# Kernel optimization log

Hardware: AMD Instinct MI355X
Metric: run time of the kernel (lower is better)

Reference implementation:

```python
import jax, jax.numpy as jnp
import numpy as np

B, S, HID = 1, 2048, 3072
NH, NKV, HD = 32, 8, 96
N_REP = NH // NKV
ROPE_THETA = 10000.0


def _rotate_half(x):
    half = x.shape[-1] // 2
    return jnp.concatenate([-x[..., half:], x[..., :half]], axis=-1)


def setup_inputs() -> dict:
    key = jax.random.key(0)
    k1, k2, k3 = jax.random.split(key, 3)
    hidden_states = jax.random.normal(k1, (B, S, HID), dtype=jnp.float32)
    qkv_w = jax.random.normal(k2, (NH * HD + 2 * NKV * HD, HID), dtype=jnp.float32) * 0.02
    o_w = jax.random.normal(k3, (HID, NH * HD), dtype=jnp.float32) * 0.02
    position_ids = jnp.broadcast_to(jnp.arange(S, dtype=jnp.int64)[None, :], (B, S))
    causal = jnp.tril(jnp.ones((S, S), dtype=bool))
    attention_mask = jnp.where(causal, 0.0, jnp.finfo(jnp.float32).min)[None, None].astype(jnp.float32)
    attention_mask = jnp.broadcast_to(attention_mask, (B, 1, S, S))
    return {"hidden_states": hidden_states, "position_ids": position_ids,
            "attention_mask": attention_mask, "qkv_w": qkv_w, "o_w": o_w}


def reference(hidden_states, position_ids, attention_mask, qkv_w, o_w):
    b, s, _ = hidden_states.shape
    qkv = jnp.einsum('bsh,oh->bso', hidden_states, qkv_w)
    q_pos = NH * HD
    q = qkv[..., :q_pos]
    k = qkv[..., q_pos:q_pos + NKV * HD]
    v = qkv[..., q_pos + NKV * HD:]
    # [b, heads, s, hd]
    q = q.reshape(b, s, NH, HD).transpose(0, 2, 1, 3)
    k = k.reshape(b, s, NKV, HD).transpose(0, 2, 1, 3)
    v = v.reshape(b, s, NKV, HD).transpose(0, 2, 1, 3)
    # RoPE
    inv_freq = 1.0 / (ROPE_THETA ** (jnp.arange(0, HD, 2, dtype=jnp.float32) / HD))
    freqs = position_ids.astype(jnp.float32)[:, :, None] * inv_freq[None, None, :]  # [b,s,hd/2]
    emb = jnp.concatenate([freqs, freqs], axis=-1)  # [b,s,hd]
    cos = jnp.cos(emb)[:, None, :, :]
    sin = jnp.sin(emb)[:, None, :, :]
    q = q * cos + _rotate_half(q) * sin
    k = k * cos + _rotate_half(k) * sin
    # GQA repeat_kv (repeat_interleave on head dim)
    k = jnp.repeat(k, N_REP, axis=1)
    v = jnp.repeat(v, N_REP, axis=1)
    scores = jnp.einsum('bhqd,bhkd->bhqk', q, k) / jnp.sqrt(jnp.float32(HD))
    scores = scores + attention_mask
    w = jax.nn.softmax(scores.astype(jnp.float32), axis=-1).astype(v.dtype)
    attn = jnp.einsum('bhqk,bhkd->bhqd', w, v)
    attn = attn.transpose(0, 2, 1, 3).reshape(b, s, NH * HD)
    out = jnp.einsum('bsf,of->bso', attn, o_w)
    return out
```

## Files before the change

kernel.cpp:

```cpp
#include <hip/hip_runtime.h>

#define S_LEN 2048
#define HID_DIM 3072
#define NH 32
#define NKV 8
#define HD 96
#define QKV_OUT 4608

typedef __attribute__((ext_vector_type(8))) short short8;
typedef __attribute__((ext_vector_type(4))) float floatx4;

__device__ __forceinline__ unsigned short f2b(float f) {
    unsigned int u = __float_as_uint(f);
    u = (u + 0x7FFFu + ((u >> 16) & 1u)) >> 16;
    return (unsigned short)u;
}
__device__ __forceinline__ float b2f(unsigned short h) {
    return __uint_as_float(((unsigned int)h) << 16);
}
__device__ __forceinline__ void async_ld16(const void* g, void* l) {
    __builtin_amdgcn_global_load_lds((const __attribute__((address_space(1))) void*)g,
                                     (__attribute__((address_space(3))) void*)l, 16, 0, 0);
}
__device__ __forceinline__ float fast_exp2(float x) {
#if __has_builtin(__builtin_amdgcn_exp2f)
    return __builtin_amdgcn_exp2f(x);
#else
    return exp2f(x);
#endif
}
__device__ __forceinline__ void store_out(float* C, size_t i, float v) { C[i] = v; }
__device__ __forceinline__ void store_out(unsigned short* C, size_t i, float v) { C[i] = f2b(v); }


__global__ void cvt3_tiled(const float* __restrict__ a, int nab,
                           const float* __restrict__ b, int nbb,
                           const float* __restrict__ c, int ncb,
                           unsigned short* __restrict__ oa,
                           unsigned short* __restrict__ ob,
                           unsigned short* __restrict__ oc) {
    int wid = blockIdx.x * 4 + (threadIdx.x >> 6);
    const int l = threadIdx.x & 63;
    const float* src;
    unsigned short* dst;
    int j = wid;
    if (j < nab) { src = a; dst = oa; }
    else {
        j -= nab;
        if (j < nbb) { src = b; dst = ob; }
        else {
            j -= nbb;
            if (j >= ncb) return;
            src = c; dst = oc;
        }
    }
    const int KB = HID_DIM >> 5;
    int rt = j / KB, kc = j - rt * KB;
    int i = l & 15, q = l >> 4;
    const float* p = src + ((size_t)rt * 16 + i) * HID_DIM + kc * 32 + q * 8;
    float4 v0 = *(const float4*)p;
    float4 v1 = *(const float4*)(p + 4);
    short8 o;
    o[0] = (short)f2b(v0.x); o[1] = (short)f2b(v0.y);
    o[2] = (short)f2b(v0.z); o[3] = (short)f2b(v0.w);
    o[4] = (short)f2b(v1.x); o[5] = (short)f2b(v1.y);
    o[6] = (short)f2b(v1.z); o[7] = (short)f2b(v1.w);
    *(short8*)(dst + (size_t)j * 512 + l * 8) = o;
}

template <typename OUT>
__global__ void gemm_bt(const unsigned short* __restrict__ A,
                        const unsigned short* __restrict__ B,
                        OUT* __restrict__ C, int M, int N, int K) {
    __shared__ unsigned short As[16 * 512];
    __shared__ unsigned short Bs[16 * 512];
    const int KB = K >> 5;
    const int t = threadIdx.x;
    const int w = t >> 6;
    const int l = t & 63;
    const int lane15 = l & 15;
    const int quad = l >> 4;
    const int rowt = blockIdx.y * 8;
    const int colt = blockIdx.x * 8;
    const int wm = (w >> 1) * 64;
    const int wn = (w & 1) * 64;

    const floatx4 vzero = {0.f, 0.f, 0.f, 0.f};
    floatx4 acc[4][4];
#pragma unroll
    for (int i = 0; i < 4; ++i)
#pragma unroll
        for (int j = 0; j < 4; ++j) acc[i][j] = vzero;

    const int xA = wm >> 4, xB = wn >> 4;
    for (int kc0 = 0; kc0 < KB; kc0 += 2) {
        __syncthreads();
#pragma unroll
        for (int j = 0; j < 4; ++j) {
            int s = w * 4 + j;
            int x = s >> 1, kkb = s & 1;
            size_t ablk = (size_t)(rowt + x) * KB + kc0 + kkb;
            size_t bblk = (size_t)(colt + x) * KB + kc0 + kkb;
            async_ld16(A + ablk * 512 + l * 8, As + s * 512 + l * 8);
            async_ld16(B + bblk * 512 + l * 8, Bs + s * 512 + l * 8);
        }
        __syncthreads();
#pragma unroll
        for (int kkb = 0; kkb < 2; ++kkb) {
            short8 af[4], bfr[4];
#pragma unroll
            for (int mi = 0; mi < 4; ++mi)
                af[mi] = *(const short8*)(As + ((xA + mi) * 2 + kkb) * 512 + l * 8);
#pragma unroll
            for (int ni = 0; ni < 4; ++ni)
                bfr[ni] = *(const short8*)(Bs + ((xB + ni) * 2 + kkb) * 512 + l * 8);
#pragma unroll
            for (int mi = 0; mi < 4; ++mi)
#pragma unroll
                for (int ni = 0; ni < 4; ++ni)
                    acc[mi][ni] = __builtin_amdgcn_mfma_f32_16x16x32_bf16(af[mi], bfr[ni], acc[mi][ni], 0, 0, 0);
        }
    }
#pragma unroll
    for (int mi = 0; mi < 4; ++mi)
#pragma unroll
        for (int ni = 0; ni < 4; ++ni)
#pragma unroll
            for (int r = 0; r < 4; ++r) {
                int m = rowt * 16 + wm + mi * 16 + quad * 4 + r;
                int n = colt * 16 + wn + ni * 16 + lane15;
                store_out(C, (size_t)m * N + n, acc[mi][ni][r]);
            }
}

__global__ void rope_split(const unsigned short* __restrict__ qkv,
                           unsigned short* __restrict__ Qd,
                           unsigned short* __restrict__ Kd,
                           unsigned short* __restrict__ Vd) {
    const int s = blockIdx.x;
    const int t = threadIdx.x;
    const unsigned short* row = qkv + (size_t)s * QKV_OUT;
    const float L2T_48 = 0.2768273412406135f;
    const float SCALE2 = 0.14724444f;

    for (int i = t; i < NH * 48; i += 256) {
        int h = i / 48, d = i - (i / 48) * 48;
        float f = (float)s * exp2f(-(float)d * L2T_48);
        float sn, cs;
        sincosf(f, &sn, &cs);
        float q1 = b2f(row[h * 96 + d]);
        float q2 = b2f(row[h * 96 + d + 48]);
        size_t base = ((size_t)h * S_LEN + s) * HD;
        Qd[base + d] = f2b((q1 * cs - q2 * sn) * SCALE2);
        Qd[base + d + 48] = f2b((q2 * cs + q1 * sn) * SCALE2);
    }
    for (int i = t; i < NKV * 48; i += 256) {
        int h = i / 48, d = i - (i / 48) * 48;
        float f = (float)s * exp2f(-(float)d * L2T_48);
        float sn, cs;
        sincosf(f, &sn, &cs);
        float k1 = b2f(row[3072 + h * 96 + d]);
        float k2 = b2f(row[3072 + h * 96 + d + 48]);
        size_t base = ((size_t)h * S_LEN + s) * HD;
        Kd[base + d] = f2b(k1 * cs - k2 * sn);
        Kd[base + d + 48] = f2b(k2 * cs + k1 * sn);
    }
    for (int i = t; i < NKV * HD; i += 256) {
        int h = i / 96, d = i - (i / 96) * 96;
        Vd[((size_t)h * S_LEN + s) * HD + d] = row[3840 + i];
    }
}

__global__ void transpose_v(const unsigned short* __restrict__ V,
                            unsigned short* __restrict__ Vt) {
    __shared__ unsigned short T[96][72];
    const int kvh = blockIdx.x >> 5;
    const int s0 = (blockIdx.x & 31) * 64;
    const int t = threadIdx.x;
#pragma unroll
    for (int it = 0; it < 3; ++it) {
        int c = it * 256 + t;
        int r = c / 12, c8 = c - r * 12;
        short8 v = *(const short8*)(V + ((size_t)kvh * S_LEN + s0 + r) * HD + c8 * 8);
#pragma unroll
        for (int j = 0; j < 8; ++j) T[c8 * 8 + j][r] = (unsigned short)v[j];
    }
    __syncthreads();
#pragma unroll
    for (int it = 0; it < 3; ++it) {
        int c = it * 256 + t;
        int d = c >> 3, c8 = c & 7;
        short8 v;
#pragma unroll
        for (int j = 0; j < 8; ++j) v[j] = (short)T[d][c8 * 8 + j];
        *(short8*)(Vt + ((size_t)kvh * HD + d) * S_LEN + s0 + c8 * 8) = v;
    }
}

#define ATTN_M0 8.0f
__global__ __launch_bounds__(256) void attn_fwd(const unsigned short* __restrict__ Q,
                                                const unsigned short* __restrict__ K,
                                                const unsigned short* __restrict__ Vt,
                                                unsigned short* __restrict__ O) {
    __shared__ unsigned short Qs[4 * 3 * 512];
    __shared__ unsigned short Ks[12 * 512];
    __shared__ unsigned short Vs[12 * 512];
    __shared__ unsigned short Ps[4][16 * 72];
    const int h = blockIdx.x;
    const int qt = (int)gridDim.y - 1 - blockIdx.y;
    const int kvh = h >> 2;
    const int q0 = qt * 64;
    const int t = threadIdx.x, w = t >> 6, l = t & 63;
    const int lane15 = l & 15, quad = l >> 4;
    unsigned short* Pw = Ps[w];

    const unsigned short* Qg = Q + ((size_t)h * S_LEN + q0) * HD;
#pragma unroll
    for (int kkb = 0; kkb < 3; ++kkb)
        async_ld16(Qg + (w * 16 + lane15) * HD + kkb * 32 + quad * 8,
                   Qs + (w * 3 + kkb) * 512 + l * 8);

    int koff[3], voff0[3];
    long vofS[3];
#pragma unroll
    for (int j = 0; j < 3; ++j) {
        int c = w * 3 + j;
        int ct = c & 3, kkb = c >> 2;
        koff[j] = (ct * 16 + lane15) * HD + kkb * 32 + quad * 8;
        int nt = c % 6, kb2 = c / 6;
        vofS[j] = (long)(nt * 16 + lane15) * S_LEN + kb2 * 32 + quad * 8;
        voff0[j] = c * 512 + l * 8;
    }

    const floatx4 vzero = {0.f, 0.f, 0.f, 0.f};
    floatx4 accO[6];
#pragma unroll
    for (int nt = 0; nt < 6; ++nt) accO[nt] = vzero;
    float lsum[4] = {0.f, 0.f, 0.f, 0.f};

    const unsigned short* Kg = K + (size_t)kvh * S_LEN * HD;
    const unsigned short* Vg = Vt + (size_t)kvh * HD * S_LEN;
    const int qrow0 = q0 + w * 16 + quad * 4;

    for (int kt = 0; kt <= qt; ++kt) {
        const int k0 = kt * 64;
        __syncthreads();
#pragma unroll
        for (int j = 0; j < 3; ++j) {
            int c = w * 3 + j;
            async_ld16(Kg + (size_t)k0 * HD + koff[j], Ks + c * 512 + l * 8);
            async_ld16(Vg + k0 + vofS[j], Vs + voff0[j]);
        }
        __syncthreads();

        floatx4 accS[4];
#pragma unroll
        for (int ct = 0; ct < 4; ++ct) accS[ct] = vzero;
#pragma unroll
        for (int kkb = 0; kkb < 3; ++kkb) {
            short8 aq = *(const short8*)(Qs + (w * 3 + kkb) * 512 + l * 8);
#pragma unroll
            for (int ct = 0; ct < 4; ++ct) {
                short8 bk = *(const short8*)(Ks + (kkb * 4 + ct) * 512 + l * 8);
                accS[ct] = __builtin_amdgcn_mfma_f32_16x16x32_bf16(aq, bk, accS[ct], 0, 0, 0);
            }
        }

        if (kt < qt) {
#pragma unroll
            for (int ct = 0; ct < 4; ++ct)
#pragma unroll
                for (int r = 0; r < 4; ++r) {
                    float p = fast_exp2(accS[ct][r] - ATTN_M0);
                    lsum[r] += p;
                    Pw[(quad * 4 + r) * 72 + ct * 16 + lane15] = f2b(p);
                }
        } else {
#pragma unroll
            for (int ct = 0; ct < 4; ++ct) {
                int kcol = k0 + ct * 16 + lane15;
#pragma unroll
                for (int r = 0; r < 4; ++r) {
                    float s = (kcol <= qrow0 + r) ? accS[ct][r] - ATTN_M0 : -1.0e30f;
                    float p = fast_exp2(s);
                    lsum[r] += p;
                    Pw[(quad * 4 + r) * 72 + ct * 16 + lane15] = f2b(p);
                }
            }
        }

#pragma unroll
        for (int kb2 = 0; kb2 < 2; ++kb2) {
            short8 ap = *(const short8*)(Pw + lane15 * 72 + kb2 * 32 + quad * 8);
#pragma unroll
            for (int nt = 0; nt < 6; ++nt) {
                short8 bv = *(const short8*)(Vs + (kb2 * 6 + nt) * 512 + l * 8);
                accO[nt] = __builtin_amdgcn_mfma_f32_16x16x32_bf16(ap, bv, accO[nt], 0, 0, 0);
            }
        }
    }

    for (int off = 1; off < 16; off <<= 1)
#pragma unroll
        for (int r = 0; r < 4; ++r) lsum[r] += __shfl_xor(lsum[r], off, 64);
    float inv[4];
#pragma unroll
    for (int r = 0; r < 4; ++r) inv[r] = 1.f / lsum[r];
    const int srow0 = q0 + w * 16 + quad * 4;
#pragma unroll
    for (int nt = 0; nt < 6; ++nt) {
        int n = h * HD + nt * 16 + lane15;
        size_t base = ((size_t)(srow0 >> 4) * (HID_DIM >> 5) + (n >> 5)) * 512
                      + ((n & 31) >> 3) * 128 + (n & 7);
#pragma unroll
        for (int r = 0; r < 4; ++r) {
            int m15 = (srow0 + r) & 15;
            O[base + m15 * 8] = f2b(accO[nt][r] * inv[r]);
        }
    }
}

extern "C" void kernel_launch(void* const* d_in, const int* in_sizes, int n_in,
                              void* d_out, int out_size, void* d_ws, size_t ws_size,
                              hipStream_t stream) {
    const float* hidden = (const float*)d_in[0];
    const float* qkv_w = (const float*)d_in[3];
    const float* o_w = (const float*)d_in[4];
    float* out = (float*)d_out;

    unsigned short* Xb = (unsigned short*)d_ws;
    unsigned short* Wq = Xb + (size_t)S_LEN * HID_DIM;
    unsigned short* Wo = Wq + (size_t)QKV_OUT * HID_DIM;
    unsigned short* QKVb = Wo + (size_t)HID_DIM * HID_DIM;
    unsigned short* Qb = QKVb + (size_t)S_LEN * QKV_OUT;
    unsigned short* Kb = Qb + (size_t)NH * S_LEN * HD;
    unsigned short* Vb = Kb + (size_t)NKV * S_LEN * HD;
    unsigned short* Ab = Vb + (size_t)NKV * S_LEN * HD;
    unsigned short* Vtb = QKVb;

    int nab = S_LEN * HID_DIM / 512, nbb = QKV_OUT * HID_DIM / 512, ncb = HID_DIM * HID_DIM / 512;
    int nblk = nab + nbb + ncb;
    cvt3_tiled<<<nblk / 4, 256, 0, stream>>>(hidden, nab, qkv_w, nbb, o_w, ncb, Xb, Wq, Wo);

    gemm_bt<unsigned short><<<dim3(QKV_OUT / 128, S_LEN / 128), 256, 0, stream>>>(
        Xb, Wq, QKVb, S_LEN, QKV_OUT, HID_DIM);
    rope_split<<<S_LEN, 256, 0, stream>>>(QKVb, Qb, Kb, Vb);
    transpose_v<<<NKV * (S_LEN / 64), 256, 0, stream>>>(Vb, Vtb);
    attn_fwd<<<dim3(NH, S_LEN / 64), 256, 0, stream>>>(Qb, Kb, Vtb, Ab);
    gemm_bt<float><<<dim3(HID_DIM / 128, S_LEN / 128), 256, 0, stream>>>(
        Ab, Wo, out, S_LEN, HID_DIM, HID_DIM);
}
```

Baseline: 353.5 us.

## Use a double-buffered 256x256 tile GEMM for the QKV projection

Adds a new gemm_pipe kernel for the QKV projection. Each block computes a 256x256 output tile with 512 threads and 128KB of dynamic LDS. Async global-to-LDS loads are double-buffered so the next K-slice is fetched while MFMAs run on the current one. The larger tile raises data reuse per LDS load, but the grid shrinks to 144 blocks, which risks leaving many CUs idle on a 256-CU part.

New measurement: 356.0 us. Within noise of the previous version (+0.7%).

```diff
diff --git a/kernel.cpp b/kernel.cpp
--- a/kernel.cpp
+++ b/kernel.cpp
@@ -68,6 +68,130 @@
     *(short8*)(dst + (size_t)j * 512 + l * 8) = o;
 }
 
+__global__ __launch_bounds__(512, 2) void gemm_pipe(const unsigned short* __restrict__ A,
+                                                    const unsigned short* __restrict__ B,
+                                                    unsigned short* __restrict__ C,
+                                                    int M, int N, int K) {
+    extern __shared__ __attribute__((aligned(16))) char smem_raw[];
+    unsigned short* lds = (unsigned short*)smem_raw;
+    const int KB = K >> 5;
+    const int NT = K >> 6;
+    const int t = threadIdx.x, w = t >> 6, l = t & 63;
+    const int lane15 = l & 15, quad = l >> 4;
+    const int wmi = w >> 2;
+    const int wni = w & 3;
+    const int rowt0 = blockIdx.y * 16;
+    const int colt0 = blockIdx.x * 16;
+
+    const floatx4 vzero = {0.f, 0.f, 0.f, 0.f};
+    floatx4 acc[8][4];
+#pragma unroll
+    for (int i = 0; i < 8; ++i)
+#pragma unroll
+        for (int j = 0; j < 4; ++j) acc[i][j] = vzero;
+
+    const unsigned short* ga[4];
+    const unsigned short* gb[4];
+    int lo[4];
+#pragma unroll
+    for (int j = 0; j < 4; ++j) {
+        int s = (w << 2) + j;
+        ga[j] = A + ((size_t)(rowt0 + (s >> 1)) * KB + (s & 1)) * 512 + l * 8;
+        gb[j] = B + ((size_t)(colt0 + (s >> 1)) * KB + (s & 1)) * 512 + l * 8;
+        lo[j] = s * 512 + l * 8;
+    }
+
+#define STAGE(T)                                                             \
+    {                                                                        \
+        unsigned short* base_ = lds + (((T) & 1) << 15);                     \
+        size_t koff_ = (size_t)(T) * 1024;                                   \
+        _Pragma("unroll")                                                    \
+        for (int j = 0; j < 4; ++j) {                                        \
+            async_ld16(ga[j] + koff_, base_ + lo[j]);                        \
+            async_ld16(gb[j] + koff_, base_ + 16384 + lo[j]);                \
+        }                                                                    \
+    }
+
+    STAGE(0);
+    for (int T = 0; T < NT; ++T) {
+        if (T + 1 < NT) {
+            STAGE(T + 1);
+            asm volatile("s_waitcnt vmcnt(8)" ::: "memory");
+        } else {
+            asm volatile("s_waitcnt vmcnt(0)" ::: "memory");
+        }
+        __builtin_amdgcn_s_barrier();
+        asm volatile("" ::: "memory");
+
+        const unsigned short* Ab = lds + ((T & 1) << 15);
+        const unsigned short* Bb = Ab + 16384;
+        short8 a[8], b0[4], b1[4];
+#pragma unroll
+        for (int mi = 0; mi < 4; ++mi)
+#pragma unroll
+            for (int kk = 0; kk < 2; ++kk)
+                a[mi * 2 + kk] = *(const short8*)(Ab + (((wmi * 8 + mi) << 1) + kk) * 512 + l * 8);
+#pragma unroll
+        for (int ni = 0; ni < 2; ++ni)
+#pragma unroll
+            for (int kk = 0; kk < 2; ++kk)
+                b0[ni * 2 + kk] = *(const short8*)(Bb + (((wni * 4 + ni) << 1) + kk) * 512 + l * 8);
+#pragma unroll
+        for (int mi = 0; mi < 4; ++mi)
+#pragma unroll
+            for (int ni = 0; ni < 2; ++ni)
+#pragma unroll
+                for (int kk = 0; kk < 2; ++kk)
+                    acc[mi][ni] = __builtin_amdgcn_mfma_f32_16x16x32_bf16(a[mi * 2 + kk], b0[ni * 2 + kk], acc[mi][ni], 0, 0, 0);
+#pragma unroll
+        for (int ni = 0; ni < 2; ++ni)
+#pragma unroll
+            for (int kk = 0; kk < 2; ++kk)
+                b1[ni * 2 + kk] = *(const short8*)(Bb + (((wni * 4 + 2 + ni) << 1) + kk) * 512 + l * 8);
+#pragma unroll
+        for (int mi = 0; mi < 4; ++mi)
+#pragma unroll
+            for (int ni = 0; ni < 2; ++ni)
+#pragma unroll
+                for (int kk = 0; kk < 2; ++kk)
+                    acc[mi][2 + ni] = __builtin_amdgcn_mfma_f32_16x16x32_bf16(a[mi * 2 + kk], b1[ni * 2 + kk], acc[mi][2 + ni], 0, 0, 0);
+#pragma unroll
+        for (int mi = 0; mi < 4; ++mi)
+#pragma unroll
+            for (int kk = 0; kk < 2; ++kk)
+                a[mi * 2 + kk] = *(const short8*)(Ab + (((wmi * 8 + 4 + mi) << 1) + kk) * 512 + l * 8);
+#pragma unroll
+        for (int mi = 0; mi < 4; ++mi)
+#pragma unroll
+            for (int ni = 0; ni < 2; ++ni)
+#pragma unroll
+                for (int kk = 0; kk < 2; ++kk)
+                    acc[4 + mi][2 + ni] = __builtin_amdgcn_mfma_f32_16x16x32_bf16(a[mi * 2 + kk], b1[ni * 2 + kk], acc[4 + mi][2 + ni], 0, 0, 0);
+#pragma unroll
+        for (int mi = 0; mi < 4; ++mi)
+#pragma unroll
+            for (int ni = 0; ni < 2; ++ni)
+#pragma unroll
+                for (int kk = 0; kk < 2; ++kk)
+                    acc[4 + mi][ni] = __builtin_amdgcn_mfma_f32_16x16x32_bf16(a[mi * 2 + kk], b0[ni * 2 + kk], acc[4 + mi][ni], 0, 0, 0);
+
+        asm volatile("" ::: "memory");
+        __builtin_amdgcn_s_barrier();
+    }
+#undef STAGE
+
+#pragma unroll
+    for (int mi = 0; mi < 8; ++mi)
+#pragma unroll
+        for (int ni = 0; ni < 4; ++ni)
+#pragma unroll
+            for (int r = 0; r < 4; ++r) {
+                int m = rowt0 * 16 + wmi * 128 + mi * 16 + quad * 4 + r;
+                int n = colt0 * 16 + wni * 64 + ni * 16 + lane15;
+                C[(size_t)m * N + n] = f2b(acc[mi][ni][r]);
+            }
+}
+
 template <typename OUT>
 __global__ void gemm_bt(const unsigned short* __restrict__ A,
                         const unsigned short* __restrict__ B,
@@ -338,11 +462,18 @@
     unsigned short* Ab = Vb + (size_t)NKV * S_LEN * HD;
     unsigned short* Vtb = QKVb;
 
+    static bool lds_init = false;
+    if (!lds_init) {
+        hipFuncSetAttribute(reinterpret_cast<const void*>(gemm_pipe),
+                            hipFuncAttributeMaxDynamicSharedMemorySize, 131072);
+        lds_init = true;
+    }
+
     int nab = S_LEN * HID_DIM / 512, nbb = QKV_OUT * HID_DIM / 512, ncb = HID_DIM * HID_DIM / 512;
     int nblk = nab + nbb + ncb;
     cvt3_tiled<<<nblk / 4, 256, 0, stream>>>(hidden, nab, qkv_w, nbb, o_w, ncb, Xb, Wq, Wo);
 
-    gemm_bt<unsigned short><<<dim3(QKV_OUT / 128, S_LEN / 128), 256, 0, stream>>>(
+    gemm_pipe<<<dim3(QKV_OUT / 256, S_LEN / 256), 512, 131072, stream>>>(
         Xb, Wq, QKVb, S_LEN, QKV_OUT, HID_DIM);
     rope_split<<<S_LEN, 256, 0, stream>>>(QKVb, Qb, Kb, Vb);
     transpose_v<<<NKV * (S_LEN / 64), 256, 0, stream>>>(Vb, Vtb);
```
